# Kernel optimization log

Hardware: AMD Instinct MI355X
Metric: run time of the kernel (lower is better)

The kernel has to match this reference:

```python
import jax, jax.numpy as jnp
import numpy as np

D_MODEL, D_FF, H, DK, DV = 1024, 4096, 16, 64, 64
B, S = 16, 512
EPS = 1e-6

def layer_norm(x, g, b):
    mu = jnp.mean(x, axis=-1, keepdims=True)
    var = jnp.var(x, axis=-1, keepdims=True)
    return (x - mu) / jnp.sqrt(var + EPS) * g + b

def setup_inputs() -> dict:
    key = jax.random.key(0)
    ks = jax.random.split(key, 16)
    def lin(k, fan_in, fan_out):
        lim = 1.0 / np.sqrt(fan_in)
        kw, kb = jax.random.split(k)
        W = jax.random.uniform(kw, (fan_in, fan_out), jnp.float32, -lim, lim)
        b = jax.random.uniform(kb, (fan_out,), jnp.float32, -lim, lim)
        return W, b
    Wq, bq = lin(ks[0], D_MODEL, DK * H)
    Wk, bk = lin(ks[1], D_MODEL, DK * H)
    Wv, bv = lin(ks[2], D_MODEL, DV * H)
    Wo, bo = lin(ks[3], DV * H, D_MODEL)
    w1, b1 = lin(ks[4], D_MODEL, D_FF)   # conv1d k=1 == pointwise linear
    w2, b2 = lin(ks[5], D_FF, D_MODEL)
    return {
        "enc_inputs": jax.random.normal(ks[6], (B, S, D_MODEL), jnp.float32),
        "Wq": Wq, "bq": bq, "Wk": Wk, "bk": bk, "Wv": Wv, "bv": bv,
        "Wo": Wo, "bo": bo,
        "ln1_g": jnp.ones((D_MODEL,), jnp.float32), "ln1_b": jnp.zeros((D_MODEL,), jnp.float32),
        "w1": w1, "b1": b1, "w2": w2, "b2": b2,
        "ln2_g": jnp.ones((D_MODEL,), jnp.float32), "ln2_b": jnp.zeros((D_MODEL,), jnp.float32),
        "mask": jax.random.randint(ks[7], (B, S), 0, 2, jnp.int32),
        "max_neighbors": S,
    }

def reference(enc_inputs, Wq, bq, Wk, bk, Wv, bv, Wo, bo, ln1_g, ln1_b,
              w1, b1, w2, b2, ln2_g, ln2_b, mask, max_neighbors):
    x = enc_inputs  # [B, S, D]
    residual = x
    # projections -> [B, H, S, d]
    q = (x @ Wq + bq).reshape(B, S, H, DK).transpose(0, 2, 1, 3)
    k = (x @ Wk + bk).reshape(B, S, H, DK).transpose(0, 2, 1, 3)
    v = (x @ Wv + bv).reshape(B, S, H, DV).transpose(0, 2, 1, 3)
    scores = jnp.einsum('bhqd,bhkd->bhqk', q, k) / np.sqrt(DK)
    pad = (mask == 0)[:, None, None, :]  # [B,1,1,S] broadcasts over heads & query
    scores = jnp.where(pad, jnp.float32(-1e9), scores)
    attn = jax.nn.softmax(scores, axis=-1)
    ctx = jnp.einsum('bhqk,bhkd->bhqd', attn, v)
    ctx = ctx.transpose(0, 2, 1, 3).reshape(B, S, H * DV)
    ctx = ctx @ Wo + bo
    ctx = layer_norm(ctx + residual, ln1_g, ln1_b)
    # position-wise FFN (conv1d kernel=1 == linear)
    ff = jax.nn.relu(ctx @ w1 + b1) @ w2 + b2
    out = layer_norm(ff + ctx, ln2_g, ln2_b)
    return out, attn
```

## Files before the change

### kernel.cpp

```cpp
#include <hip/hip_runtime.h>
#include <hip/hip_bf16.h>

typedef unsigned short u16;
typedef __bf16 bf16x8 __attribute__((ext_vector_type(8)));
typedef float f32x4 __attribute__((ext_vector_type(4)));

static __device__ __forceinline__ float b2f(u16 x) {
    unsigned int u = ((unsigned int)x) << 16;
    float f; __builtin_memcpy(&f, &u, 4); return f;
}
static __device__ __forceinline__ float b2f_u32(unsigned int u) {
    float f; __builtin_memcpy(&f, &u, 4); return f;
}
static __device__ __forceinline__ u16 f2b(float f) {
    unsigned int u; __builtin_memcpy(&u, &f, 4);
    unsigned int lsb = (u >> 16) & 1u;
    u += 0x7fffu + lsb;
    return (u16)(u >> 16);
}

static __device__ __forceinline__ void gload16(const u16* g, u16* l) {
    __builtin_amdgcn_global_load_lds(
        (const __attribute__((address_space(1))) unsigned int*)g,
        (__attribute__((address_space(3))) unsigned int*)l, 16, 0, 0);
}

__global__ __launch_bounds__(256) void transpose_f2b(const float* __restrict__ src,
                                                     u16* __restrict__ dst,
                                                     int R, int C) {
    __shared__ u16 tile[32][33];
    int c0 = blockIdx.x * 32, r0 = blockIdx.y * 32;
    int tx = threadIdx.x & 31, ty = threadIdx.x >> 5;
    for (int i = ty; i < 32; i += 8) {
        int r = r0 + i, c = c0 + tx;
        tile[i][tx] = (r < R && c < C) ? f2b(src[(long)r * C + c]) : (u16)0;
    }
    __syncthreads();
    for (int i = ty; i < 32; i += 8) {
        int c = c0 + i, r = r0 + tx;
        if (c < C && r < R) dst[(long)c * R + r] = tile[tx][i];
    }
}

__global__ __launch_bounds__(256) void concat3(const float* a, const float* b, const float* c,
                                               float* out) {
    int i = blockIdx.x * 256 + threadIdx.x;
    if (i < 1024) out[i] = a[i];
    else if (i < 2048) out[i] = b[i - 1024];
    else if (i < 3072) out[i] = c[i - 2048];
}

__global__ __launch_bounds__(256) void conv_f2b(const float* __restrict__ src,
                                                u16* __restrict__ dst, long n) {
    long i = ((long)blockIdx.x * 256 + threadIdx.x) * 4;
    if (i >= n) return;
    float4 f = *(const float4*)(src + i);
    ushort4 o;
    o.x = f2b(f.x); o.y = f2b(f.y); o.z = f2b(f.z); o.w = f2b(f.w);
    *(ushort4*)(dst + i) = o;
}

#define BM 128
#define BN 128
#define BK 32
__global__ __launch_bounds__(256) void gemm_bt(
    const u16* __restrict__ A, const u16* __restrict__ B,
    const float* __restrict__ bias, u16* __restrict__ C,
    int M, int N, int K, int lda, int ldb, int ldc, int relu) {
    __shared__ __align__(16) u16 As[BM][BK];
    __shared__ __align__(16) u16 Bs[BN][BK];

    int m0 = blockIdx.y * BM;
    int n0 = blockIdx.x * BN;
    int tid = threadIdx.x;
    int lane = tid & 63;
    int wave = tid >> 6;
    int wm = (wave >> 1) * 64;
    int wn = (wave & 1) * 64;
    int lrow = lane & 15;
    int quad = lane >> 4;

    f32x4 acc[4][4];
#pragma unroll
    for (int i = 0; i < 4; i++)
#pragma unroll
        for (int j = 0; j < 4; j++) acc[i][j] = (f32x4){0.f, 0.f, 0.f, 0.f};

    const u16* Arow = A + (long)m0 * lda;
    const u16* Brow = B + (long)n0 * ldb;

    for (int k0 = 0; k0 < K; k0 += BK) {
#pragma unroll
        for (int i = 0; i < 2; i++) {
            int idx = (i * 4 + wave) * 64 + lane;
            int row = idx >> 2;
            int seg = (idx & 3) * 8;
            gload16(Arow + (long)row * lda + k0 + seg, &As[0][0] + (i * 4 + wave) * 512);
            gload16(Brow + (long)row * ldb + k0 + seg, &Bs[0][0] + (i * 4 + wave) * 512);
        }
        __syncthreads();

        bf16x8 af[4], bfr[4];
#pragma unroll
        for (int mi = 0; mi < 4; mi++)
            af[mi] = *(const bf16x8*)&As[wm + mi * 16 + lrow][quad * 8];
#pragma unroll
        for (int ni = 0; ni < 4; ni++)
            bfr[ni] = *(const bf16x8*)&Bs[wn + ni * 16 + lrow][quad * 8];
#pragma unroll
        for (int mi = 0; mi < 4; mi++)
#pragma unroll
            for (int ni = 0; ni < 4; ni++)
                acc[mi][ni] = __builtin_amdgcn_mfma_f32_16x16x32_bf16(
                    af[mi], bfr[ni], acc[mi][ni], 0, 0, 0);
        __syncthreads();
    }

#pragma unroll
    for (int mi = 0; mi < 4; mi++) {
        int r0w = m0 + wm + mi * 16 + quad * 4;
#pragma unroll
        for (int ni = 0; ni < 4; ni++) {
            int col = n0 + wn + ni * 16 + lrow;
            float bv = bias ? bias[col] : 0.f;
#pragma unroll
            for (int r = 0; r < 4; r++) {
                float v = acc[mi][ni][r] + bv;
                if (relu) v = fmaxf(v, 0.f);
                C[(long)(r0w + r) * ldc + col] = f2b(v);
            }
        }
    }
}

__global__ __launch_bounds__(256) void split_v(const u16* __restrict__ qkv,
                                               u16* __restrict__ vT) {
    __shared__ u16 tile[32][33];
    int bh = blockIdx.z;
    int b = bh >> 4, h = bh & 15;
    int s0 = blockIdx.x * 32;
    int d0 = blockIdx.y * 32;
    int tx = threadIdx.x & 31, ty = threadIdx.x >> 5;
    for (int i = ty; i < 32; i += 8)
        tile[i][tx] = qkv[((long)(b * 512 + s0 + i)) * 3072 + 2048 + h * 64 + d0 + tx];
    __syncthreads();
    for (int i = ty; i < 32; i += 8)
        vT[((long)bh * 64 + d0 + i) * 512 + s0 + tx] = tile[tx][i];
}

__global__ __launch_bounds__(256) void attn_fused(
    const u16* __restrict__ qkv, const u16* __restrict__ vT,
    const int* __restrict__ mask, float* __restrict__ attnOut,
    u16* __restrict__ ctx) {
    __shared__ __align__(16) u16 s_tile[128][72];
    __shared__ __align__(16) u16 s_p[4][16][136];
    __shared__ unsigned long long m_bits[8];

    int id = blockIdx.x;
    int t_ = id >> 3;
    int mtile = t_ & 7;
    int bh = (id & 7) + ((t_ >> 3) << 3);
    int b = bh >> 4, h = bh & 15;
    int tid = threadIdx.x, lane = tid & 63, wave = tid >> 6;
    int lrow = lane & 15, quad = lane >> 4;
    int m0 = mtile * 64;

    const u16* Qbase = qkv + (long)(b * 512) * 3072 + h * 64;
    const u16* Kbase = Qbase + 1024;

    {
        int i0 = wave * 64 + lane;
        unsigned long long bl0 = __ballot(mask[b * 512 + i0] != 0);
        if (lane == 0) m_bits[wave] = bl0;
        unsigned long long bl1 = __ballot(mask[b * 512 + 256 + i0] != 0);
        if (lane == 0) m_bits[4 + wave] = bl1;
    }

#pragma unroll
    for (int i = 0; i < 2; i++) {
        int idx = i * 256 + tid;
        int r = idx >> 3, c = (idx & 7) * 8;
        *(uint4*)&s_tile[r][c] = *(const uint4*)(Qbase + (long)(m0 + r) * 3072 + c);
    }
    __syncthreads();
    bf16x8 qf[2];
    qf[0] = *(const bf16x8*)&s_tile[wave * 16 + lrow][0 + quad * 8];
    qf[1] = *(const bf16x8*)&s_tile[wave * 16 + lrow][32 + quad * 8];
    __syncthreads();

    f32x4 sacc[32];
#pragma unroll
    for (int t = 0; t < 32; t++) sacc[t] = (f32x4){0.f, 0.f, 0.f, 0.f};

    for (int nc = 0; nc < 4; nc++) {
#pragma unroll
        for (int i = 0; i < 4; i++) {
            int idx = i * 256 + tid;
            int r = idx >> 3, c = (idx & 7) * 8;
            *(uint4*)&s_tile[r][c] = *(const uint4*)(Kbase + (long)(nc * 128 + r) * 3072 + c);
        }
        __syncthreads();
#pragma unroll
        for (int ni = 0; ni < 8; ni++) {
            bf16x8 b0 = *(const bf16x8*)&s_tile[ni * 16 + lrow][0 + quad * 8];
            bf16x8 b1 = *(const bf16x8*)&s_tile[ni * 16 + lrow][32 + quad * 8];
            int t = nc * 8 + ni;
            sacc[t] = __builtin_amdgcn_mfma_f32_16x16x32_bf16(qf[0], b0, sacc[t], 0, 0, 0);
            sacc[t] = __builtin_amdgcn_mfma_f32_16x16x32_bf16(qf[1], b1, sacc[t], 0, 0, 0);
        }
        __syncthreads();
    }

    float mx[4] = {-3.0e38f, -3.0e38f, -3.0e38f, -3.0e38f};
#pragma unroll
    for (int t = 0; t < 32; t++) {
        int col = t * 16 + lrow;
        int on = (int)((m_bits[col >> 6] >> (col & 63)) & 1ull);
#pragma unroll
        for (int r = 0; r < 4; r++) {
            float s = on ? sacc[t][r] * 0.125f : -1e9f;
            sacc[t][r] = s;
            mx[r] = fmaxf(mx[r], s);
        }
    }
#pragma unroll
    for (int off = 1; off < 16; off <<= 1)
#pragma unroll
        for (int r = 0; r < 4; r++) mx[r] = fmaxf(mx[r], __shfl_xor(mx[r], off));
    float sm[4] = {0.f, 0.f, 0.f, 0.f};
#pragma unroll
    for (int t = 0; t < 32; t++)
#pragma unroll
        for (int r = 0; r < 4; r++) {
            float e = __expf(sacc[t][r] - mx[r]);
            sacc[t][r] = e;
            sm[r] += e;
        }
#pragma unroll
    for (int off = 1; off < 16; off <<= 1)
#pragma unroll
        for (int r = 0; r < 4; r++) sm[r] += __shfl_xor(sm[r], off);
#pragma unroll
    for (int r = 0; r < 4; r++) sm[r] = 1.0f / sm[r];
#pragma unroll
    for (int t = 0; t < 32; t++)
#pragma unroll
        for (int r = 0; r < 4; r++) sacc[t][r] *= sm[r];

    f32x4 cacc[4];
#pragma unroll
    for (int ni = 0; ni < 4; ni++) cacc[ni] = (f32x4){0.f, 0.f, 0.f, 0.f};
    const u16* vh = vT + (long)bh * 64 * 512;
    int prr = lane >> 5;
    int pcc = lane & 31;

    for (int nc = 0; nc < 4; nc++) {
#pragma unroll
        for (int t2 = 0; t2 < 8; t2++) {
            int t = nc * 8 + t2;
#pragma unroll
            for (int r = 0; r < 4; r++)
                s_p[wave][quad * 4 + r][t2 * 16 + lrow] = f2b(sacc[t][r]);
        }
        __syncthreads();

        {
            float* abase = attnOut + (long)bh * 512 * 512
                         + (long)(m0 + wave * 16) * 512 + nc * 128;
#pragma unroll
            for (int i = 0; i < 8; i++) {
                int row = i * 2 + prr;
                uint2 pv = *(const uint2*)&s_p[wave][row][pcc * 4];
                float4 o;
                o.x = b2f_u32(pv.x << 16);
                o.y = b2f_u32(pv.x & 0xffff0000u);
                o.z = b2f_u32(pv.y << 16);
                o.w = b2f_u32(pv.y & 0xffff0000u);
                *(float4*)(abase + (long)row * 512 + pcc * 4) = o;
            }
        }

#pragma unroll
        for (int kk = 0; kk < 4; kk++) {
            bf16x8 pf = *(const bf16x8*)&s_p[wave][lrow][kk * 32 + quad * 8];
#pragma unroll
            for (int ni = 0; ni < 4; ni++) {
                bf16x8 vf = *(const bf16x8*)(vh + (long)(ni * 16 + lrow) * 512 + nc * 128 + kk * 32 + quad * 8);
                cacc[ni] = __builtin_amdgcn_mfma_f32_16x16x32_bf16(pf, vf, cacc[ni], 0, 0, 0);
            }
        }
    }

    u16* crow = ctx + (long)(b * 512 + m0 + wave * 16 + quad * 4) * 1024 + h * 64 + lrow;
#pragma unroll
    for (int ni = 0; ni < 4; ni++)
#pragma unroll
        for (int r = 0; r < 4; r++) crow[(long)r * 1024 + ni * 16] = f2b(cacc[ni][r]);
}

__global__ __launch_bounds__(256) void add_ln(const u16* __restrict__ a,
                                              const void* __restrict__ r, int r_fp32,
                                              const float* __restrict__ g,
                                              const float* __restrict__ beta,
                                              void* __restrict__ out, int out_fp32) {
    long row = blockIdx.x;
    const u16* pa = a + row * 1024;
    int tid = threadIdx.x;
    float v[4];
    float sum = 0.f, sq = 0.f;
#pragma unroll
    for (int j = 0; j < 4; j++) {
        int c = tid + j * 256;
        float rv = r_fp32 ? ((const float*)r)[row * 1024 + c]
                          : b2f(((const u16*)r)[row * 1024 + c]);
        float x = b2f(pa[c]) + rv;
        v[j] = x;
        sum += x;
        sq += x * x;
    }
#pragma unroll
    for (int off = 32; off >= 1; off >>= 1) {
        sum += __shfl_xor(sum, off);
        sq += __shfl_xor(sq, off);
    }
    __shared__ float red[2][4];
    int wave = tid >> 6, lane = tid & 63;
    if (lane == 0) { red[0][wave] = sum; red[1][wave] = sq; }
    __syncthreads();
    sum = red[0][0] + red[0][1] + red[0][2] + red[0][3];
    sq = red[1][0] + red[1][1] + red[1][2] + red[1][3];
    float mu = sum * (1.f / 1024.f);
    float var = sq * (1.f / 1024.f) - mu * mu;
    float rstd = rsqrtf(var + 1e-6f);
#pragma unroll
    for (int j = 0; j < 4; j++) {
        int c = tid + j * 256;
        float y = (v[j] - mu) * rstd * g[c] + beta[c];
        if (out_fp32) ((float*)out)[row * 1024 + c] = y;
        else ((u16*)out)[row * 1024 + c] = f2b(y);
    }
}

extern "C" void kernel_launch(void* const* d_in, const int* in_sizes, int n_in,
                              void* d_out, int out_size, void* d_ws, size_t ws_size,
                              hipStream_t stream) {
    const float* x   = (const float*)d_in[0];
    const float* Wq  = (const float*)d_in[1];
    const float* bq  = (const float*)d_in[2];
    const float* Wk  = (const float*)d_in[3];
    const float* bk  = (const float*)d_in[4];
    const float* Wv  = (const float*)d_in[5];
    const float* bv  = (const float*)d_in[6];
    const float* Wo  = (const float*)d_in[7];
    const float* bo  = (const float*)d_in[8];
    const float* g1  = (const float*)d_in[9];
    const float* be1 = (const float*)d_in[10];
    const float* w1  = (const float*)d_in[11];
    const float* b1  = (const float*)d_in[12];
    const float* w2  = (const float*)d_in[13];
    const float* b2  = (const float*)d_in[14];
    const float* g2  = (const float*)d_in[15];
    const float* be2 = (const float*)d_in[16];
    const int* mask  = (const int*)d_in[17];

    float* out = (float*)d_out;
    float* attn = out + (long)8192 * 1024;

    char* w = (char*)d_ws;
    auto alloc = [&](size_t bytes) {
        char* p = w;
        w += (bytes + 255) & ~(size_t)255;
        return p;
    };
    u16* WqkvT = (u16*)alloc(3072L * 1024 * 2);
    u16* WoT   = (u16*)alloc(1024L * 1024 * 2);
    u16* w1T   = (u16*)alloc(4096L * 1024 * 2);
    u16* w2T   = (u16*)alloc(1024L * 4096 * 2);
    float* bqkv = (float*)alloc(3072L * 4);
    u16* xb    = (u16*)alloc(8192L * 1024 * 2);
    char* P1 = alloc(8192L * 4096 * 2);
    u16* qkv = (u16*)P1;
    u16* ff  = (u16*)P1;
    char* P2 = alloc(256L * 64 * 512 * 2);
    u16* vT = (u16*)P2;
    u16* y2 = (u16*)P2;
    u16* ctx = (u16*)alloc(8192L * 1024 * 2);
    u16* x1  = (u16*)alloc(8192L * 1024 * 2);
    u16* y   = (u16*)alloc(8192L * 1024 * 2);

    dim3 blk(256);

    transpose_f2b<<<dim3(32, 32), blk, 0, stream>>>(Wq, WqkvT, 1024, 1024);
    transpose_f2b<<<dim3(32, 32), blk, 0, stream>>>(Wk, WqkvT + 1024L * 1024, 1024, 1024);
    transpose_f2b<<<dim3(32, 32), blk, 0, stream>>>(Wv, WqkvT + 2048L * 1024, 1024, 1024);
    transpose_f2b<<<dim3(32, 32), blk, 0, stream>>>(Wo, WoT, 1024, 1024);
    transpose_f2b<<<dim3(128, 32), blk, 0, stream>>>(w1, w1T, 1024, 4096);
    transpose_f2b<<<dim3(32, 128), blk, 0, stream>>>(w2, w2T, 4096, 1024);
    concat3<<<12, blk, 0, stream>>>(bq, bk, bv, bqkv);
    conv_f2b<<<8192, blk, 0, stream>>>(x, xb, 8192L * 1024);

    gemm_bt<<<dim3(24, 64), blk, 0, stream>>>(
        xb, WqkvT, bqkv, qkv, 8192, 3072, 1024, 1024, 1024, 3072, 0);

    split_v<<<dim3(16, 2, 256), blk, 0, stream>>>(qkv, vT);

    attn_fused<<<dim3(2048), blk, 0, stream>>>(qkv, vT, mask, attn, ctx);

    gemm_bt<<<dim3(8, 64), blk, 0, stream>>>(
        ctx, WoT, bo, y, 8192, 1024, 1024, 1024, 1024, 1024, 0);

    add_ln<<<8192, blk, 0, stream>>>(y, x, 1, g1, be1, x1, 0);

    gemm_bt<<<dim3(32, 64), blk, 0, stream>>>(
        x1, w1T, b1, ff, 8192, 4096, 1024, 1024, 1024, 4096, 1);

    gemm_bt<<<dim3(8, 64), blk, 0, stream>>>(
        ff, w2T, b2, y2, 8192, 1024, 4096, 4096, 4096, 1024, 0);

    add_ln<<<8192, blk, 0, stream>>>(y2, x1, 0, g2, be2, out, 1);
}
```

Baseline: 897.2 us.

## Add 256x256-tile pipelined GEMM kernel for QKV and FFN1 projections

```diff
diff --git a/kernel.cpp b/kernel.cpp
--- a/kernel.cpp
+++ b/kernel.cpp
@@ -131,6 +131,151 @@
             }
         }
     }
+}
+
+__global__ __launch_bounds__(512, 1) void gemm_bt256(
+    const u16* __restrict__ A, const u16* __restrict__ B,
+    const float* __restrict__ bias, u16* __restrict__ C,
+    int M, int N, int K, int lda, int ldb, int ldc, int relu, int nbx) {
+    __shared__ __align__(16) u16 lds[2][4][8192];
+
+    int nwg = gridDim.x;
+    int id = blockIdx.x;
+    int swz = (id & 7) * (nwg >> 3) + (id >> 3);
+    int bx = swz % nbx, by = swz / nbx;
+    long m0 = (long)by * 256, n0 = (long)bx * 256;
+
+    int tid = threadIdx.x, lane = tid & 63, wave = tid >> 6;
+    int lrow = lane & 15, quad = lane >> 4;
+    int wm2 = wave >> 2;
+    int wn2 = wave & 3;
+
+    int laneRd = (lrow * 64 + quad * 16) ^ (((lrow >> 3) & 1) << 5);
+    int Sl = (lane * 16) ^ (((lane >> 5) & 1) << 5);
+    int wr = (Sl >> 6) & 15;
+    int wb = Sl & 63;
+
+    f32x4 acc[8][4];
+#pragma unroll
+    for (int i = 0; i < 8; i++)
+#pragma unroll
+        for (int j = 0; j < 4; j++) acc[i][j] = (f32x4){0.f, 0.f, 0.f, 0.f};
+    bf16x8 af[4][2], bfr[2][2];
+
+#define STAGE_HT(nb, ht, kt) do {                                              \
+    const char* _gb = ((ht) < 2)                                               \
+        ? (const char*)(A + (m0 + (ht) * 128) * lda)                           \
+        : (const char*)(B + (n0 + ((ht) - 2) * 128) * ldb);                    \
+    long _ld = (long)(((ht) < 2) ? lda : ldb) * 2;                             \
+    _Pragma("unroll")                                                          \
+    for (int j = 0; j < 2; j++) {                                              \
+        int sub = j * 8 + wave;                                                \
+        int srow = (sub >> 1) * 16 + wr;                                       \
+        int scolb = (sub & 1) * 64 + wb;                                       \
+        gload16((const u16*)(_gb + (long)srow * _ld + (long)(kt) * 128 + scolb),\
+                &lds[nb][ht][sub << 9]);                                       \
+    }                                                                          \
+} while (0)
+
+#define DSLOAD_A(qm) do {                                                      \
+    const char* _p = _ab + ((qm) << 14);                                       \
+    _Pragma("unroll") for (int mi = 0; mi < 4; mi++)                           \
+    _Pragma("unroll") for (int kk = 0; kk < 2; kk++)                           \
+        af[mi][kk] = *(const bf16x8*)(_p + ((mi * 4 + kk) << 10));             \
+} while (0)
+
+#define DSLOAD_B(qn) do {                                                      \
+    const char* _p = _bb + ((qn) << 14);                                       \
+    _Pragma("unroll") for (int ni = 0; ni < 2; ni++)                           \
+    _Pragma("unroll") for (int kk = 0; kk < 2; kk++)                           \
+        bfr[ni][kk] = *(const bf16x8*)(_p + ((ni * 8 + kk) << 10));            \
+} while (0)
+
+#define DOMFMA(qm, qn) do {                                                    \
+    __builtin_amdgcn_s_setprio(1);                                             \
+    _Pragma("unroll") for (int mi = 0; mi < 4; mi++)                           \
+    _Pragma("unroll") for (int ni = 0; ni < 2; ni++)                           \
+    _Pragma("unroll") for (int kk = 0; kk < 2; kk++)                           \
+        acc[(qm) * 4 + mi][(qn) * 2 + ni] =                                    \
+            __builtin_amdgcn_mfma_f32_16x16x32_bf16(                           \
+                af[mi][kk], bfr[ni][kk], acc[(qm) * 4 + mi][(qn) * 2 + ni],    \
+                0, 0, 0);                                                      \
+    __builtin_amdgcn_s_setprio(0);                                             \
+} while (0)
+
+#define MIDBAR()  do { __builtin_amdgcn_s_barrier(); __builtin_amdgcn_sched_barrier(0); } while (0)
+#define ENDBAR()  do { __builtin_amdgcn_sched_barrier(0); __builtin_amdgcn_s_barrier(); } while (0)
+
+    int NT = K >> 6;
+    STAGE_HT(0, 0, 0);
+    STAGE_HT(0, 2, 0);
+    STAGE_HT(0, 1, 0);
+    STAGE_HT(0, 3, 0);
+
+    for (int t = 0; t < NT - 1; t++) {
+        int cur = t & 1, nxt = cur ^ 1;
+        const char* _ab = (const char*)&lds[cur][0][0] + (wm2 << 11) + laneRd;
+        const char* _bb = (const char*)&lds[cur][2][0] + (wn2 << 11) + laneRd;
+        STAGE_HT(nxt, 0, t + 1);
+        asm volatile("s_waitcnt vmcnt(6)" ::: "memory");
+        MIDBAR();
+        DSLOAD_A(0); DSLOAD_B(0); DOMFMA(0, 0);
+        ENDBAR();
+        STAGE_HT(nxt, 2, t + 1);
+        asm volatile("s_waitcnt vmcnt(6)" ::: "memory");
+        MIDBAR();
+        DSLOAD_A(1); DOMFMA(1, 0);
+        ENDBAR();
+        STAGE_HT(nxt, 1, t + 1);
+        asm volatile("s_waitcnt vmcnt(6)" ::: "memory");
+        MIDBAR();
+        DSLOAD_B(1); DOMFMA(1, 1);
+        ENDBAR();
+        STAGE_HT(nxt, 3, t + 1);
+        MIDBAR();
+        DSLOAD_A(0); DOMFMA(0, 1);
+        ENDBAR();
+    }
+    {
+        int cur = (NT - 1) & 1;
+        const char* _ab = (const char*)&lds[cur][0][0] + (wm2 << 11) + laneRd;
+        const char* _bb = (const char*)&lds[cur][2][0] + (wn2 << 11) + laneRd;
+        asm volatile("s_waitcnt vmcnt(4)" ::: "memory");
+        MIDBAR();
+        DSLOAD_A(0); DSLOAD_B(0); DOMFMA(0, 0);
+        ENDBAR();
+        asm volatile("s_waitcnt vmcnt(2)" ::: "memory");
+        MIDBAR();
+        DSLOAD_A(1); DOMFMA(1, 0);
+        ENDBAR();
+        asm volatile("s_waitcnt vmcnt(0)" ::: "memory");
+        MIDBAR();
+        DSLOAD_B(1); DOMFMA(1, 1);
+        ENDBAR();
+        DSLOAD_A(0); DOMFMA(0, 1);
+    }
+
+#pragma unroll
+    for (int mg = 0; mg < 8; mg++) {
+        long row0 = m0 + (long)(((mg >> 2) * 8 + (mg & 3) * 2 + wm2) * 16 + quad * 4);
+#pragma unroll
+        for (int ng = 0; ng < 4; ng++) {
+            long col = n0 + ((ng >> 1) * 8 + (ng & 1) * 4 + wn2) * 16 + lrow;
+            float bv = bias ? bias[col] : 0.f;
+#pragma unroll
+            for (int r = 0; r < 4; r++) {
+                float v = acc[mg][ng][r] + bv;
+                if (relu) v = fmaxf(v, 0.f);
+                C[(row0 + r) * ldc + col] = f2b(v);
+            }
+        }
+    }
+#undef STAGE_HT
+#undef DSLOAD_A
+#undef DSLOAD_B
+#undef DOMFMA
+#undef MIDBAR
+#undef ENDBAR
 }
 
 __global__ __launch_bounds__(256) void split_v(const u16* __restrict__ qkv,
@@ -399,8 +544,8 @@
     concat3<<<12, blk, 0, stream>>>(bq, bk, bv, bqkv);
     conv_f2b<<<8192, blk, 0, stream>>>(x, xb, 8192L * 1024);
 
-    gemm_bt<<<dim3(24, 64), blk, 0, stream>>>(
-        xb, WqkvT, bqkv, qkv, 8192, 3072, 1024, 1024, 1024, 3072, 0);
+    gemm_bt256<<<dim3(384), dim3(512), 0, stream>>>(
+        xb, WqkvT, bqkv, qkv, 8192, 3072, 1024, 1024, 1024, 3072, 0, 12);
 
     split_v<<<dim3(16, 2, 256), blk, 0, stream>>>(qkv, vT);
 
@@ -411,8 +556,8 @@
 
     add_ln<<<8192, blk, 0, stream>>>(y, x, 1, g1, be1, x1, 0);
 
-    gemm_bt<<<dim3(32, 64), blk, 0, stream>>>(
-        x1, w1T, b1, ff, 8192, 4096, 1024, 1024, 1024, 4096, 1);
+    gemm_bt256<<<dim3(512), dim3(512), 0, stream>>>(
+        x1, w1T, b1, ff, 8192, 4096, 1024, 1024, 1024, 4096, 1, 16);
 
     gemm_bt<<<dim3(8, 64), blk, 0, stream>>>(
         ff, w2T, b2, y2, 8192, 1024, 4096, 4096, 4096, 1024, 0);
```

New measurement: 864.1 us. 1.04x faster.
